# Performance work log

Measured on AMD Instinct MI355X. Metric: run time of the kernel, lower is better.

Reference implementation:

```python
import jax, jax.numpy as jnp
import numpy as np

B, K, C, L = 16, 8, 64, 2048
OFFSET = 2.0  # self.offset in Coupling
EPS = 1e-7    # clamp for logit stability (flows' safe_log analogue)


def setup_inputs() -> dict:
    key = jax.random.key(0)
    ks = jax.random.split(key, 6)
    return {
        "x_change": jax.random.normal(ks[0], (B, C, L), jnp.float32),
        "a": jax.random.normal(ks[1], (B, C, L), jnp.float32),
        "b": jax.random.normal(ks[2], (B, C, L), jnp.float32),
        "pi": jax.random.normal(ks[3], (B, K, C, L), jnp.float32),
        "mu": jax.random.normal(ks[4], (B, K, C, L), jnp.float32),
        "s": jax.random.normal(ks[5], (B, K, C, L), jnp.float32) * 0.1,  # log-scales
        "sldj": jnp.zeros((B,), jnp.float32),
    }


def reference(x_change, a, b, pi, mu, s, sldj):
    # scale = sigmoid(a + offset) + (1 - sigmoid(offset))
    sig_off = 1.0 - jax.nn.sigmoid(jnp.float32(OFFSET))
    scale = jax.nn.sigmoid(a + OFFSET) + sig_off                      # [B,C,L]

    logpi = jax.nn.log_softmax(pi, axis=1)                            # [B,K,C,L]
    z = (x_change[:, None] - mu) * jnp.exp(-s)                        # [B,K,C,L]

    # logistic.mixture_log_cdf: logsumexp_k(log pi_k + log sigmoid(z_k))
    log_cdf = jax.scipy.special.logsumexp(logpi + jax.nn.log_sigmoid(z), axis=1)
    u = jnp.clip(jnp.exp(log_cdf), EPS, 1.0 - EPS)                    # [B,C,L]

    # logistic.inverse (forward): logit, with ldj = -log(u) - log(1-u)
    y = jnp.log(u) - jnp.log1p(-u)
    scale_ldj = -jnp.log(u) - jnp.log1p(-u)

    # logistic.mixture_log_pdf: logsumexp_k(log pi_k + z - s - 2 softplus(z))
    log_pdf = jax.scipy.special.logsumexp(
        logpi + z - s - 2.0 * jax.nn.softplus(z), axis=1)             # [B,C,L]

    sldj_out = sldj + jnp.sum(
        (log_pdf + scale_ldj + jnp.log(scale)).reshape(sldj.shape[0], -1), axis=-1)
    out = (y + b) * scale                                             # [B,C,L]
    return out, sldj_out
```

## Files before the change

kernel.cpp:

```cpp
#include <hip/hip_runtime.h>

#define BB 16
#define KK 8
#define CC 64
#define LL 2048

constexpr int CL = CC * LL;
constexpr int QUADS_PER_BATCH = CL / 4;
constexpr int NBLOCKS = (BB * QUADS_PER_BATCH) / 256;

#define SIG_OFF 0.11920292202211755f
#define LOG_EPS -16.11809565095832f

__device__ __forceinline__ float frcp(float x) { return __builtin_amdgcn_rcpf(x); }

__device__ __forceinline__ float get4(const float4& v, int e) {
    switch (e) {
        case 0: return v.x;
        case 1: return v.y;
        case 2: return v.z;
        default: return v.w;
    }
}

__device__ __forceinline__ void set4(float4& v, int e, float f) {
    switch (e) {
        case 0: v.x = f; break;
        case 1: v.y = f; break;
        case 2: v.z = f; break;
        default: v.w = f; break;
    }
}

__global__ void init_sldj_kernel(const float* __restrict__ sldj_in,
                                 float* __restrict__ sldj_out) {
    int i = threadIdx.x;
    if (i < BB) sldj_out[i] = sldj_in[i];
}

__global__ __launch_bounds__(256) void coupling_kernel(
    const float* __restrict__ x,
    const float* __restrict__ a,
    const float* __restrict__ bv,
    const float* __restrict__ pi,
    const float* __restrict__ mu,
    const float* __restrict__ s,
    float* __restrict__ out,
    float* __restrict__ sldj_out) {

    const int idx = blockIdx.x * 256 + threadIdx.x;
    const int b   = idx >> 15;
    const int rem = idx & (QUADS_PER_BATCH - 1);
    const int base = b * CL + rem * 4;

    const float4 x4 = *(const float4*)(x + base);
    const float4 a4 = *(const float4*)(a + base);
    const float4 b4 = *(const float4*)(bv + base);

    float Spi[4] = {0.f, 0.f, 0.f, 0.f};
    float Nc[4]  = {0.f, 0.f, 0.f, 0.f};
    float N1[4]  = {0.f, 0.f, 0.f, 0.f};
    float Np[4]  = {0.f, 0.f, 0.f, 0.f};

#pragma unroll
    for (int k = 0; k < KK; ++k) {
        const int kb = (b * KK + k) * CL + rem * 4;
        const float4 pi4 = *(const float4*)(pi + kb);
        const float4 mu4 = *(const float4*)(mu + kb);
        const float4 s4  = *(const float4*)(s  + kb);

#pragma unroll
        for (int e = 0; e < 4; ++e) {
            const float p      = get4(pi4, e);
            const float m      = get4(mu4, e);
            const float sk     = get4(s4, e);
            const float invstd = __expf(-sk);
            const float z      = (get4(x4, e) - m) * invstd;

            const float t  = __expf(-fabsf(z));
            const float r  = frcp(1.f + t);
            const float tr = t * r;
            const float sig  = (z >= 0.f) ? r  : tr;
            const float osig = (z >= 0.f) ? tr : r;

            const float ek = __expf(p);
            Spi[e] += ek;
            Nc[e]  += ek * sig;
            N1[e]  += ek * osig;
            Np[e]  += ek * invstd * sig * osig;
        }
    }

    float contrib = 0.f;
    float4 out4;

#pragma unroll
    for (int e = 0; e < 4; ++e) {
        const float lSpi = __logf(Spi[e]);
        const float lu   = fmaxf(__logf(Nc[e]) - lSpi, LOG_EPS);
        const float lomu = fmaxf(__logf(N1[e]) - lSpi, LOG_EPS);
        const float y        = lu - lomu;
        const float ldj_term = -lu - lomu;
        const float log_pdf  = __logf(Np[e]) - lSpi;

        const float ae = get4(a4, e) + 2.f;
        const float t2 = __expf(-fabsf(ae));
        const float r2 = frcp(1.f + t2);
        const float sc = ((ae >= 0.f) ? r2 : t2 * r2) + SIG_OFF;

        set4(out4, e, (y + get4(b4, e)) * sc);
        contrib += log_pdf + ldj_term + __logf(sc);
    }

    *(float4*)(out + base) = out4;

#pragma unroll
    for (int off = 32; off > 0; off >>= 1)
        contrib += __shfl_down(contrib, off, 64);

    __shared__ float wsum[4];
    const int lane = threadIdx.x & 63;
    const int wid  = threadIdx.x >> 6;
    if (lane == 0) wsum[wid] = contrib;
    __syncthreads();
    if (threadIdx.x == 0) {
        atomicAdd(&sldj_out[b], wsum[0] + wsum[1] + wsum[2] + wsum[3]);
    }
}

extern "C" void kernel_launch(void* const* d_in, const int* in_sizes, int n_in,
                              void* d_out, int out_size, void* d_ws, size_t ws_size,
                              hipStream_t stream) {
    const float* x    = (const float*)d_in[0];
    const float* a    = (const float*)d_in[1];
    const float* bv   = (const float*)d_in[2];
    const float* pi   = (const float*)d_in[3];
    const float* mu   = (const float*)d_in[4];
    const float* s    = (const float*)d_in[5];
    const float* sldj = (const float*)d_in[6];

    float* out      = (float*)d_out;
    float* sldj_out = out + (size_t)BB * CL;

    init_sldj_kernel<<<1, 64, 0, stream>>>(sldj, sldj_out);
    coupling_kernel<<<NBLOCKS, 256, 0, stream>>>(x, a, bv, pi, mu, s, out, sldj_out);
}
```

Baseline: 231.9 us.

## Process one element per thread with all K loads issued upfront

Each thread now handles one element instead of four, so the grid grows fourfold, and vectorized float4 accesses become scalar coalesced loads. All 24 pi/mu/s loads are hoisted ahead of the compute, with a sched_barrier so the compiler keeps them there, and launch bounds request 8 blocks per CU for higher occupancy. The aim is more memory-level parallelism and latency hiding for a bandwidth-bound kernel. In exchange it loses 128-bit loads and issues four times as many reduction atomics.

```diff
diff --git a/kernel.cpp b/kernel.cpp
--- a/kernel.cpp
+++ b/kernel.cpp
@@ -6,31 +6,13 @@
 #define LL 2048
 
 constexpr int CL = CC * LL;
-constexpr int QUADS_PER_BATCH = CL / 4;
-constexpr int NBLOCKS = (BB * QUADS_PER_BATCH) / 256;
+constexpr int NELEM = BB * CL;
+constexpr int NBLOCKS = NELEM / 256;
 
 #define SIG_OFF 0.11920292202211755f
 #define LOG_EPS -16.11809565095832f
 
 __device__ __forceinline__ float frcp(float x) { return __builtin_amdgcn_rcpf(x); }
-
-__device__ __forceinline__ float get4(const float4& v, int e) {
-    switch (e) {
-        case 0: return v.x;
-        case 1: return v.y;
-        case 2: return v.z;
-        default: return v.w;
-    }
-}
-
-__device__ __forceinline__ void set4(float4& v, int e, float f) {
-    switch (e) {
-        case 0: v.x = f; break;
-        case 1: v.y = f; break;
-        case 2: v.z = f; break;
-        default: v.w = f; break;
-    }
-}
 
 __global__ void init_sldj_kernel(const float* __restrict__ sldj_in,
                                  float* __restrict__ sldj_out) {
@@ -38,7 +20,7 @@
     if (i < BB) sldj_out[i] = sldj_in[i];
 }
 
-__global__ __launch_bounds__(256) void coupling_kernel(
+__global__ __launch_bounds__(256, 8) void coupling_kernel(
     const float* __restrict__ x,
     const float* __restrict__ a,
     const float* __restrict__ bv,
@@ -49,70 +31,58 @@
     float* __restrict__ sldj_out) {
 
     const int idx = blockIdx.x * 256 + threadIdx.x;
-    const int b   = idx >> 15;
-    const int rem = idx & (QUADS_PER_BATCH - 1);
-    const int base = b * CL + rem * 4;
+    const int b   = idx >> 17;
+    const int kbase = (b << 20) + (idx & (CL - 1));
 
-    const float4 x4 = *(const float4*)(x + base);
-    const float4 a4 = *(const float4*)(a + base);
-    const float4 b4 = *(const float4*)(bv + base);
+    const float xe = x[idx];
+    const float ae = a[idx];
+    const float be = bv[idx];
 
-    float Spi[4] = {0.f, 0.f, 0.f, 0.f};
-    float Nc[4]  = {0.f, 0.f, 0.f, 0.f};
-    float N1[4]  = {0.f, 0.f, 0.f, 0.f};
-    float Np[4]  = {0.f, 0.f, 0.f, 0.f};
+    float pv[KK], mv[KK], sv[KK];
+#pragma unroll
+    for (int k = 0; k < KK; ++k) {
+        const int o = kbase + k * CL;
+        pv[k] = pi[o];
+        mv[k] = mu[o];
+        sv[k] = s[o];
+    }
+    __builtin_amdgcn_sched_barrier(0);
+
+    float Spi = 0.f, Nc = 0.f, N1 = 0.f, Np = 0.f;
 
 #pragma unroll
     for (int k = 0; k < KK; ++k) {
-        const int kb = (b * KK + k) * CL + rem * 4;
-        const float4 pi4 = *(const float4*)(pi + kb);
-        const float4 mu4 = *(const float4*)(mu + kb);
-        const float4 s4  = *(const float4*)(s  + kb);
+        const float invstd = __expf(-sv[k]);
+        const float z      = (xe - mv[k]) * invstd;
 
-#pragma unroll
-        for (int e = 0; e < 4; ++e) {
-            const float p      = get4(pi4, e);
-            const float m      = get4(mu4, e);
-            const float sk     = get4(s4, e);
-            const float invstd = __expf(-sk);
-            const float z      = (get4(x4, e) - m) * invstd;
+        const float t  = __expf(-fabsf(z));
+        const float r  = frcp(1.f + t);
+        const float tr = t * r;
+        const float sig  = (z >= 0.f) ? r  : tr;
+        const float osig = (z >= 0.f) ? tr : r;
 
-            const float t  = __expf(-fabsf(z));
-            const float r  = frcp(1.f + t);
-            const float tr = t * r;
-            const float sig  = (z >= 0.f) ? r  : tr;
-            const float osig = (z >= 0.f) ? tr : r;
-
-            const float ek = __expf(p);
-            Spi[e] += ek;
-            Nc[e]  += ek * sig;
-            N1[e]  += ek * osig;
-            Np[e]  += ek * invstd * sig * osig;
-        }
+        const float ek = __expf(pv[k]);
+        Spi += ek;
+        Nc  += ek * sig;
+        N1  += ek * osig;
+        Np  += ek * invstd * sig * osig;
     }
 
-    float contrib = 0.f;
-    float4 out4;
+    const float lSpi = __logf(Spi);
+    const float lu   = fmaxf(__logf(Nc) - lSpi, LOG_EPS);
+    const float lomu = fmaxf(__logf(N1) - lSpi, LOG_EPS);
+    const float y        = lu - lomu;
+    const float ldj_term = -lu - lomu;
+    const float log_pdf  = __logf(Np) - lSpi;
 
-#pragma unroll
-    for (int e = 0; e < 4; ++e) {
-        const float lSpi = __logf(Spi[e]);
-        const float lu   = fmaxf(__logf(Nc[e]) - lSpi, LOG_EPS);
-        const float lomu = fmaxf(__logf(N1[e]) - lSpi, LOG_EPS);
-        const float y        = lu - lomu;
-        const float ldj_term = -lu - lomu;
-        const float log_pdf  = __logf(Np[e]) - lSpi;
+    const float av = ae + 2.f;
+    const float t2 = __expf(-fabsf(av));
+    const float r2 = frcp(1.f + t2);
+    const float sc = ((av >= 0.f) ? r2 : t2 * r2) + SIG_OFF;
 
-        const float ae = get4(a4, e) + 2.f;
-        const float t2 = __expf(-fabsf(ae));
-        const float r2 = frcp(1.f + t2);
-        const float sc = ((ae >= 0.f) ? r2 : t2 * r2) + SIG_OFF;
+    out[idx] = (y + be) * sc;
 
-        set4(out4, e, (y + get4(b4, e)) * sc);
-        contrib += log_pdf + ldj_term + __logf(sc);
-    }
-
-    *(float4*)(out + base) = out4;
+    float contrib = log_pdf + ldj_term + __logf(sc);
 
 #pragma unroll
     for (int off = 32; off > 0; off >>= 1)
@@ -140,7 +110,7 @@
     const float* sldj = (const float*)d_in[6];
 
     float* out      = (float*)d_out;
-    float* sldj_out = out + (size_t)BB * CL;
+    float* sldj_out = out + (size_t)NELEM;
 
     init_sldj_kernel<<<1, 64, 0, stream>>>(sldj, sldj_out);
     coupling_kernel<<<NBLOCKS, 256, 0, stream>>>(x, a, bv, pi, mu, s, out, sldj_out);
```

Result: slower. 260.7 us (+12.4%).
